# Kernel tuning notes

Hardware: AMD Instinct MI355X
Metric: run time of the kernel (lower is better)

Reference implementation:

```python
import jax
import jax.numpy as jnp
import numpy as np

NB_FEATURES = 512
DIM_EXPLOSION_FACTOR = 20
MB_DIM = NB_FEATURES * DIM_EXPLOSION_FACTOR  # 10240
NB_PROJ_ENTRIES = 6   # nonzeros per row of the random projection
HASH_LENGTH = 32      # k for k-winner-take-all
NB_CLASSES = 100
BATCH = 8192


def _make_rand_proj(key):
    # Sparse binary projection: each MB neuron samples NB_PROJ_ENTRIES inputs.
    r = jax.random.uniform(key, (MB_DIM, NB_FEATURES), dtype=jnp.float32)
    th = jax.lax.top_k(r, NB_PROJ_ENTRIES)[0][:, -1:]  # per-row k-th largest
    return (r >= th).astype(jnp.float32)  # [MB_DIM, NB_FEATURES], ~6 ones/row


def setup_inputs() -> dict:
    key = jax.random.key(0)
    k1, k2, k3, k4 = jax.random.split(key, 4)
    x = jax.random.normal(k1, (BATCH, NB_FEATURES), dtype=jnp.float32)
    w1 = _make_rand_proj(k2)
    # PositiveLinear params (kaiming-uniform-ish scale)
    bound = 1.0 / np.sqrt(MB_DIM)
    w2 = jax.random.uniform(k3, (NB_CLASSES, MB_DIM), dtype=jnp.float32,
                            minval=-bound, maxval=bound)
    b2 = jax.random.uniform(k4, (NB_CLASSES,), dtype=jnp.float32,
                            minval=-bound, maxval=bound)
    return {"x": x, "w1": w1, "w2": w2, "b2": b2}


def reference(x, w1, w2, b2):
    # MB projection: dense matmul with the (non-learned) random projection.
    h = jnp.einsum("bf,mf->bm", x, w1)  # [B, MB_DIM]
    # k-winner-take-all sparsify: keep the HASH_LENGTH largest values per row.
    th = jax.lax.top_k(h, HASH_LENGTH)[0][:, -1:]  # k-th largest per row
    h = jnp.where(h >= th, h, jnp.zeros((), h.dtype))
    # PositiveLinear: weights clamped to min=0 before the linear.
    w2c = jnp.maximum(w2, 0.0)
    return jnp.einsum("bm,cm->bc", h, w2c) + b2  # [B, NB_CLASSES]
```

## Files before the change

kernel.cpp:

```cpp
#include <hip/hip_runtime.h>
#include <stdint.h>

typedef unsigned int uint;
typedef unsigned short ushort;

#define NB_FEATURES 512
#define MB_DIM      10240
#define NB_CLASSES  100
#define BATCH       8192
#define KSEL        32
#define VPT         40

static __device__ __forceinline__ uint f2key(float f) {
    uint u = __float_as_uint(f);
    return u ^ (0x80000000u | (uint)((int)u >> 31));
}
static __device__ __forceinline__ float key2f(uint k) {
    uint u = k ^ (0x80000000u | (uint)(((int)~k) >> 31));
    return __uint_as_float(u);
}

__global__ __launch_bounds__(256) void k_extract(const float* __restrict__ w1,
                                                 ushort* __restrict__ idx) {
    const int gw   = (blockIdx.x * 256 + threadIdx.x) >> 6;
    const int lane = threadIdx.x & 63;
    if (gw >= MB_DIM) return;
    const float* row = w1 + (size_t)gw * NB_FEATURES;
    const float4 a = *(const float4*)(row + lane * 8);
    const float4 b = *(const float4*)(row + lane * 8 + 4);
    const float v[8] = {a.x, a.y, a.z, a.w, b.x, b.y, b.z, b.w};
    int cnt = 0;
#pragma unroll
    for (int j = 0; j < 8; ++j) cnt += (v[j] > 0.5f);
    int p = cnt;
#pragma unroll
    for (int off = 1; off < 64; off <<= 1) {
        int n = __shfl_up(p, off, 64);
        if (lane >= off) p += n;
    }
    const int total = __shfl(p, 63, 64);
    int slot = p - cnt;
    ushort* dst = idx + (size_t)gw * 8;
#pragma unroll
    for (int j = 0; j < 8; ++j) {
        if (v[j] > 0.5f) {
            if (slot < 8) dst[slot] = (ushort)(lane * 8 + j);
            slot++;
        }
    }
    if (lane >= total && lane < 8) dst[lane] = (ushort)NB_FEATURES;
}

__global__ __launch_bounds__(256) void k_w2t(const float* __restrict__ w2,
                                             float* __restrict__ w2t) {
    const int i = blockIdx.x * 256 + threadIdx.x;
    if (i >= NB_CLASSES * MB_DIM) return;
    const int c = i / MB_DIM;
    const int m = i - c * MB_DIM;
    w2t[(size_t)m * NB_CLASSES + c] = fmaxf(w2[i], 0.0f);
}

template <bool USE_W2T>
__global__ __launch_bounds__(256) void k_main(
    const float* __restrict__ x, const ushort* __restrict__ idx,
    const float* __restrict__ w2t, const float* __restrict__ w2,
    const float* __restrict__ b2, float* __restrict__ out)
{
    __shared__ float xs[NB_FEATURES + 4];
    __shared__ uint  cand[512];
    __shared__ uint  s_wsum[4];
    __shared__ uint  s_piv[4];
    __shared__ uint  s_thkey;
    __shared__ uint  s_cnt1;
    __shared__ uint  s_pref;
    __shared__ int   s_k;
    __shared__ uint  list_m[64];
    __shared__ float list_v[64];

    const int tid  = threadIdx.x;
    const int lane = tid & 63;
    const int wid  = tid >> 6;
    const int brow = blockIdx.x;

    {
        const float2 v = *(const float2*)(x + (size_t)brow * NB_FEATURES + tid * 2);
        *(float2*)(xs + tid * 2) = v;
        if (tid < 4) xs[NB_FEATURES + tid] = 0.0f;
    }
    __syncthreads();

    uint key[VPT];
#pragma unroll
    for (int i = 0; i < VPT; ++i) {
        const int m = tid + (i << 8);
        const uint4 q = *(const uint4*)(idx + ((size_t)m << 3));
        float s = xs[q.x & 0xFFFFu] + xs[q.x >> 16]
                + xs[q.y & 0xFFFFu] + xs[q.y >> 16]
                + xs[q.z & 0xFFFFu] + xs[q.z >> 16]
                + xs[q.w & 0xFFFFu] + xs[q.w >> 16];
        key[i] = f2key(s);
    }

    {
        uint v = key[0];
#pragma unroll
        for (int i = 1; i < VPT; ++i) v = max(v, key[i]);
#pragma unroll
        for (int k = 2; k <= 64; k <<= 1) {
#pragma unroll
            for (int j = k >> 1; j > 0; j >>= 1) {
                const uint pr = __shfl_xor(v, j, 64);
                const bool lower = (lane & j) == 0;
                const bool asc   = (lane & k) == 0;
                const uint mn = min(v, pr), mx = max(v, pr);
                v = (lower == asc) ? mx : mn;
            }
        }
        if (lane == 31) s_piv[wid] = v;
    }
    __syncthreads();
    const uint pivot = max(max(s_piv[0], s_piv[1]), max(s_piv[2], s_piv[3]));

    int myc = 0;
#pragma unroll
    for (int i = 0; i < VPT; ++i) myc += (key[i] >= pivot) ? 1 : 0;
    int p = myc;
#pragma unroll
    for (int off = 1; off < 64; off <<= 1) {
        int n = __shfl_up(p, off, 64);
        if (lane >= off) p += n;
    }
    if (lane == 63) s_wsum[wid] = (uint)p;
    __syncthreads();
    int base = p - myc;
    for (int w = 0; w < wid; ++w) base += (int)s_wsum[w];
    const int ctot = (int)(s_wsum[0] + s_wsum[1] + s_wsum[2] + s_wsum[3]);
    {
        int slot = base;
#pragma unroll
        for (int i = 0; i < VPT; ++i) {
            if (key[i] >= pivot) {
                if (slot < 512) cand[slot] = key[i];
                slot++;
            }
        }
    }
    __syncthreads();

    if (ctot <= 512) {
        if (tid < ctot) {
            const uint u = cand[tid];
            int rank = 0;
            for (int j = 0; j < ctot; ++j) {
                const uint vv = cand[j];
                rank += ((vv > u) || (vv == u && j < tid)) ? 1 : 0;
            }
            if (rank == KSEL - 1) s_thkey = u;
        }
    } else {
        if (tid == 0) { s_pref = 0u; s_k = KSEL; }
        __syncthreads();
        for (int bit = 31; bit >= 0; --bit) {
            const uint bmask = 1u << bit;
            const uint dmask = (bit == 31) ? 0u : (0xFFFFFFFFu << (bit + 1));
            const uint pref = s_pref;
            int mc = 0;
#pragma unroll
            for (int i = 0; i < VPT; ++i)
                mc += (((key[i] & dmask) == pref) && (key[i] & bmask)) ? 1 : 0;
            if (tid == 0) s_cnt1 = 0;
            __syncthreads();
            if (mc) atomicAdd(&s_cnt1, (uint)mc);
            __syncthreads();
            if (tid == 0) {
                if ((int)s_cnt1 >= s_k) s_pref = pref | bmask;
                else s_k -= (int)s_cnt1;
            }
            __syncthreads();
        }
        if (tid == 0) s_thkey = s_pref;
    }
    __syncthreads();
    const uint thkey = s_thkey;

    int kc = 0;
#pragma unroll
    for (int i = 0; i < VPT; ++i) kc += (key[i] >= thkey) ? 1 : 0;
    int p2 = kc;
#pragma unroll
    for (int off = 1; off < 64; off <<= 1) {
        int n = __shfl_up(p2, off, 64);
        if (lane >= off) p2 += n;
    }
    if (lane == 63) s_wsum[wid] = (uint)p2;
    __syncthreads();
    int kbase = p2 - kc;
    for (int w = 0; w < wid; ++w) kbase += (int)s_wsum[w];
    const int ktot = (int)(s_wsum[0] + s_wsum[1] + s_wsum[2] + s_wsum[3]);
    {
        int slot = kbase;
#pragma unroll
        for (int i = 0; i < VPT; ++i) {
            if (key[i] >= thkey) {
                if (slot < 64) {
                    list_m[slot] = (uint)(tid + (i << 8));
                    list_v[slot] = key2f(key[i]);
                }
                slot++;
            }
        }
    }
    __syncthreads();

    const int cnt = ktot < 64 ? ktot : 64;
    if (tid < NB_CLASSES) {
        float acc = b2[tid];
        for (int j = 0; j < cnt; ++j) {
            const uint m = list_m[j];
            const float w = USE_W2T ? w2t[(size_t)m * NB_CLASSES + tid]
                                    : fmaxf(w2[(size_t)tid * MB_DIM + m], 0.0f);
            acc = fmaf(list_v[j], w, acc);
        }
        out[(size_t)brow * NB_CLASSES + tid] = acc;
    }
}

extern "C" void kernel_launch(void* const* d_in, const int* in_sizes, int n_in,
                              void* d_out, int out_size, void* d_ws, size_t ws_size,
                              hipStream_t stream) {
    const float* x  = (const float*)d_in[0];
    const float* w1 = (const float*)d_in[1];
    const float* w2 = (const float*)d_in[2];
    const float* b2 = (const float*)d_in[3];
    float* out = (float*)d_out;

    ushort* idx = (ushort*)d_ws;
    const size_t W2T_OFF = 262144;
    float* w2t = (float*)((char*)d_ws + W2T_OFF);
    const bool use_w2t =
        ws_size >= W2T_OFF + (size_t)MB_DIM * NB_CLASSES * sizeof(float);

    k_extract<<<(MB_DIM * 64) / 256, 256, 0, stream>>>(w1, idx);
    if (use_w2t) {
        k_w2t<<<(MB_DIM * NB_CLASSES + 255) / 256, 256, 0, stream>>>(w2, w2t);
        k_main<true><<<BATCH, 256, 0, stream>>>(x, idx, w2t, w2, b2, out);
    } else {
        k_main<false><<<BATCH, 256, 0, stream>>>(x, idx, nullptr, w2, b2, out);
    }
}
```

Baseline: 158.3 us.

## Replicate x across LDS banks and pack projection indices into 10-bit fields

The input row is copied 32 times into LDS, with each copy pinned to one bank by its lane slot, so the random gathers for the sparse projection avoid bank conflicts. Projection indices are packed into a uint2 holding six 10-bit entries plus an overflow flag, which drops the padded gathers. The main kernel moves to 512 threads with half the values per thread. In exchange, the roughly 66KB LDS footprint limits blocks per CU, and each block pays extra LDS stores to build the replicated copies.

```diff
diff --git a/kernel.cpp b/kernel.cpp
--- a/kernel.cpp
+++ b/kernel.cpp
@@ -9,7 +9,8 @@
 #define NB_CLASSES  100
 #define BATCH       8192
 #define KSEL        32
-#define VPT         40
+#define NTHR        512
+#define VPT         20
 
 static __device__ __forceinline__ uint f2key(float f) {
     uint u = __float_as_uint(f);
@@ -21,10 +22,13 @@
 }
 
 __global__ __launch_bounds__(256) void k_extract(const float* __restrict__ w1,
-                                                 ushort* __restrict__ idx) {
+                                                 uint2* __restrict__ idx2,
+                                                 uint* __restrict__ ovf) {
+    __shared__ ushort scr[4][8];
     const int gw   = (blockIdx.x * 256 + threadIdx.x) >> 6;
     const int lane = threadIdx.x & 63;
-    if (gw >= MB_DIM) return;
+    const int wid  = (threadIdx.x >> 6) & 3;
+
     const float* row = w1 + (size_t)gw * NB_FEATURES;
     const float4 a = *(const float4*)(row + lane * 8);
     const float4 b = *(const float4*)(row + lane * 8 + 4);
@@ -40,15 +44,27 @@
     }
     const int total = __shfl(p, 63, 64);
     int slot = p - cnt;
-    ushort* dst = idx + (size_t)gw * 8;
+
+    if (lane < 8) scr[wid][lane] = (ushort)NB_FEATURES;
+    __syncthreads();
 #pragma unroll
     for (int j = 0; j < 8; ++j) {
         if (v[j] > 0.5f) {
-            if (slot < 8) dst[slot] = (ushort)(lane * 8 + j);
+            if (slot < 8) scr[wid][slot] = (ushort)(lane * 8 + j);
             slot++;
         }
     }
-    if (lane >= total && lane < 8) dst[lane] = (ushort)NB_FEATURES;
+    __syncthreads();
+    if (lane == 0) {
+        const uint c0 = scr[wid][0], c1 = scr[wid][1], c2 = scr[wid][2];
+        const uint c3 = scr[wid][3], c4 = scr[wid][4], c5 = scr[wid][5];
+        const uint c6 = scr[wid][6], c7 = scr[wid][7];
+        uint2 q;
+        q.x = c0 | (c1 << 10) | (c2 << 20);
+        q.y = c3 | (c4 << 10) | (c5 << 20) | (total > 6 ? 0x80000000u : 0u);
+        idx2[gw] = q;
+        ovf[gw]  = c6 | (c7 << 10);
+    }
 }
 
 __global__ __launch_bounds__(256) void k_w2t(const float* __restrict__ w2,
@@ -61,15 +77,16 @@
 }
 
 template <bool USE_W2T>
-__global__ __launch_bounds__(256) void k_main(
-    const float* __restrict__ x, const ushort* __restrict__ idx,
-    const float* __restrict__ w2t, const float* __restrict__ w2,
-    const float* __restrict__ b2, float* __restrict__ out)
+__global__ __launch_bounds__(NTHR) void k_main(
+    const float* __restrict__ x, const uint2* __restrict__ idx2,
+    const uint* __restrict__ ovf, const float* __restrict__ w2t,
+    const float* __restrict__ w2, const float* __restrict__ b2,
+    float* __restrict__ out)
 {
-    __shared__ float xs[NB_FEATURES + 4];
+    __shared__ float xrep[513 * 32];
     __shared__ uint  cand[512];
-    __shared__ uint  s_wsum[4];
-    __shared__ uint  s_piv[4];
+    __shared__ uint  s_wsum[8];
+    __shared__ uint  s_piv[8];
     __shared__ uint  s_thkey;
     __shared__ uint  s_cnt1;
     __shared__ uint  s_pref;
@@ -83,21 +100,34 @@
     const int brow = blockIdx.x;
 
     {
-        const float2 v = *(const float2*)(x + (size_t)brow * NB_FEATURES + tid * 2);
-        *(float2*)(xs + tid * 2) = v;
-        if (tid < 4) xs[NB_FEATURES + tid] = 0.0f;
-    }
-    __syncthreads();
+        const float xv = x[(size_t)brow * NB_FEATURES + tid];
+        const int base = tid << 5;
+#pragma unroll
+        for (int c = 0; c < 32; ++c) {
+            xrep[base + ((c + tid) & 31)] = xv;
+        }
+        if (tid < 32) xrep[(NB_FEATURES << 5) + tid] = 0.0f;
+    }
+    __syncthreads();
+
+    const uint bb = (uint)(tid & 31);
 
     uint key[VPT];
 #pragma unroll
     for (int i = 0; i < VPT; ++i) {
-        const int m = tid + (i << 8);
-        const uint4 q = *(const uint4*)(idx + ((size_t)m << 3));
-        float s = xs[q.x & 0xFFFFu] + xs[q.x >> 16]
-                + xs[q.y & 0xFFFFu] + xs[q.y >> 16]
-                + xs[q.z & 0xFFFFu] + xs[q.z >> 16]
-                + xs[q.w & 0xFFFFu] + xs[q.w >> 16];
+        const int m = tid + (i << 9);
+        const uint2 q = idx2[m];
+        float s = xrep[((q.x & 1023u) << 5) | bb]
+                + xrep[(((q.x >> 10) & 1023u) << 5) | bb]
+                + xrep[(((q.x >> 20) & 1023u) << 5) | bb]
+                + xrep[((q.y & 1023u) << 5) | bb]
+                + xrep[(((q.y >> 10) & 1023u) << 5) | bb]
+                + xrep[(((q.y >> 20) & 1023u) << 5) | bb];
+        if (q.y & 0x80000000u) {
+            const uint o = ovf[m];
+            s += xrep[((o & 1023u) << 5) | bb]
+               + xrep[(((o >> 10) & 1023u) << 5) | bb];
+        }
         key[i] = f2key(s);
     }
 
@@ -119,7 +149,9 @@
         if (lane == 31) s_piv[wid] = v;
     }
     __syncthreads();
-    const uint pivot = max(max(s_piv[0], s_piv[1]), max(s_piv[2], s_piv[3]));
+    uint pivot = s_piv[0];
+#pragma unroll
+    for (int w = 1; w < 8; ++w) pivot = max(pivot, s_piv[w]);
 
     int myc = 0;
 #pragma unroll
@@ -134,7 +166,9 @@
     __syncthreads();
     int base = p - myc;
     for (int w = 0; w < wid; ++w) base += (int)s_wsum[w];
-    const int ctot = (int)(s_wsum[0] + s_wsum[1] + s_wsum[2] + s_wsum[3]);
+    int ctot = 0;
+#pragma unroll
+    for (int w = 0; w < 8; ++w) ctot += (int)s_wsum[w];
     {
         int slot = base;
 #pragma unroll
@@ -196,14 +230,16 @@
     __syncthreads();
     int kbase = p2 - kc;
     for (int w = 0; w < wid; ++w) kbase += (int)s_wsum[w];
-    const int ktot = (int)(s_wsum[0] + s_wsum[1] + s_wsum[2] + s_wsum[3]);
+    int ktot = 0;
+#pragma unroll
+    for (int w = 0; w < 8; ++w) ktot += (int)s_wsum[w];
     {
         int slot = kbase;
 #pragma unroll
         for (int i = 0; i < VPT; ++i) {
             if (key[i] >= thkey) {
                 if (slot < 64) {
-                    list_m[slot] = (uint)(tid + (i << 8));
+                    list_m[slot] = (uint)(tid + (i << 9));
                     list_v[slot] = key2f(key[i]);
                 }
                 slot++;
@@ -234,17 +270,18 @@
     const float* b2 = (const float*)d_in[3];
     float* out = (float*)d_out;
 
-    ushort* idx = (ushort*)d_ws;
-    const size_t W2T_OFF = 262144;
+    uint2* idx2 = (uint2*)d_ws;
+    uint*  ovf  = (uint*)((char*)d_ws + 81920);
+    const size_t W2T_OFF = 131072;
     float* w2t = (float*)((char*)d_ws + W2T_OFF);
     const bool use_w2t =
         ws_size >= W2T_OFF + (size_t)MB_DIM * NB_CLASSES * sizeof(float);
 
-    k_extract<<<(MB_DIM * 64) / 256, 256, 0, stream>>>(w1, idx);
+    k_extract<<<(MB_DIM * 64) / 256, 256, 0, stream>>>(w1, idx2, ovf);
     if (use_w2t) {
         k_w2t<<<(MB_DIM * NB_CLASSES + 255) / 256, 256, 0, stream>>>(w2, w2t);
-        k_main<true><<<BATCH, 256, 0, stream>>>(x, idx, w2t, w2, b2, out);
+        k_main<true><<<BATCH, NTHR, 0, stream>>>(x, idx2, ovf, w2t, w2, b2, out);
     } else {
-        k_main<false><<<BATCH, 256, 0, stream>>>(x, idx, nullptr, w2, b2, out);
-    }
-}
+        k_main<false><<<BATCH, NTHR, 0, stream>>>(x, idx2, ovf, nullptr, w2, b2, out);
+    }
+}
```

Result: slower. 363.1 us (+129.5%).
